# Kernel optimization log

Hardware: AMD Instinct MI355X
Metric: run time of the kernel (lower is better)

The kernel has to match this reference:

```python
import jax, jax.numpy as jnp
import numpy as np

N, E, G = 50000, 800000, 128   # nodes, edges, graphs per batch
IN, HID, OUT = 128, 256, 10
EPS = 1e-5


def setup_inputs() -> dict:
    key = jax.random.key(0)
    ks = jax.random.split(key, 12)

    def w(k, shape, fan_in):
        return jax.random.normal(k, shape, jnp.float32) * np.float32(1.0 / np.sqrt(fan_in))

    H2 = HID // 2
    return {
        "n_feat": jax.random.normal(ks[0], (N, IN), jnp.float32),
        "src": jax.random.randint(ks[1], (E,), 0, N, dtype=jnp.int32),
        "dst": jax.random.randint(ks[2], (E,), 0, N, dtype=jnp.int32),
        "graph_ids": jnp.sort(jax.random.randint(ks[3], (N,), 0, G, dtype=jnp.int32)),
        "W1": w(ks[4], (IN, HID), IN), "b1": jnp.zeros((HID,), jnp.float32),
        "W2": w(ks[5], (HID, H2), HID), "b2": jnp.zeros((H2,), jnp.float32),
        "W3": w(ks[6], (H2, H2), H2), "b3": jnp.zeros((H2,), jnp.float32),
        "Wf1": w(ks[7], (H2, H2), H2), "bf1": jnp.zeros((H2,), jnp.float32),
        "Wf2": w(ks[8], (H2, OUT), H2), "bf2": jnp.zeros((OUT,), jnp.float32),
        "gamma": jnp.ones((H2,), jnp.float32),
        "beta": jnp.zeros((H2,), jnp.float32),
    }


def _graph_conv(x, W, b, src, dst, out_dis, in_dis):
    # DGL GraphConv, norm='both': D_dst^{-1/2} A D_src^{-1/2} X W + b
    h = x * out_dis[:, None]                                   # [N, d]
    agg = jax.ops.segment_sum(h[src], dst, num_segments=N)     # scatter-add over edges
    agg = agg * in_dis[:, None]
    return agg @ W + b


def reference(n_feat, src, dst, graph_ids,
              W1, b1, W2, b2, W3, b3, Wf1, bf1, Wf2, bf2, gamma, beta):
    ones_e = jnp.ones((E,), jnp.float32)
    out_deg = jax.ops.segment_sum(ones_e, src, num_segments=N)
    in_deg = jax.ops.segment_sum(ones_e, dst, num_segments=N)
    out_dis = jax.lax.rsqrt(jnp.clip(out_deg, 1.0))   # degree clamped to min 1
    in_dis = jax.lax.rsqrt(jnp.clip(in_deg, 1.0))

    x = jax.nn.relu(_graph_conv(n_feat, W1, b1, src, dst, out_dis, in_dis))
    x = jax.nn.relu(_graph_conv(x, W2, b2, src, dst, out_dis, in_dis))
    x = jax.nn.relu(_graph_conv(x, W3, b3, src, dst, out_dis, in_dis))

    # SumPooling readout -> [G, HID//2]
    embedding = jax.ops.segment_sum(x, graph_ids, num_segments=G)

    # BatchNorm1d (training-mode batch stats, biased variance)
    mean = jnp.mean(embedding, axis=0)
    var = jnp.mean((embedding - mean) ** 2, axis=0)
    bn = (embedding - mean) * jax.lax.rsqrt(var + EPS) * gamma + beta

    h = jax.nn.relu(bn @ Wf1 + bf1)
    logits = h @ Wf2 + bf2
    return embedding, jax.nn.log_softmax(logits, axis=-1)
```

## Files before the change

### kernel.cpp

```cpp
#include <hip/hip_runtime.h>

#define N_NODES 50000
#define N_EDGES 800000
#define N_GRAPHS 128
#define IN_DIM 128
#define HID 256
#define H2 128
#define OUT_DIM 10
#define BN_EPS 1e-5f

#define NBUCK 196
#define K1_ITEMS 2048
#define NB_EDGE ((N_EDGES + K1_ITEMS - 1) / K1_ITEMS)
#define BND_BLOCKS ((N_NODES + 255) / 256)
#define CW1_BLOCKS  ((IN_DIM * HID) / 256)
#define CW2_BLOCKS  ((HID * H2) / 256)
#define CW3_BLOCKS  ((H2 * H2) / 256)

typedef __attribute__((ext_vector_type(8))) short short8_t;
typedef __attribute__((ext_vector_type(4))) float f32x4;

__device__ __forceinline__ unsigned short f2bf(float f) {
    union { float f; unsigned u; } x; x.f = f;
    unsigned r = x.u + 0x7fffu + ((x.u >> 16) & 1u);
    return (unsigned short)(r >> 16);
}
__device__ __forceinline__ float bf2f(unsigned short h) {
    union { unsigned u; float f; } x; x.u = ((unsigned)h) << 16;
    return x.f;
}
__device__ __forceinline__ unsigned pack2(float a, float b) {
    return (unsigned)f2bf(a) | ((unsigned)f2bf(b) << 16);
}

__device__ __forceinline__ void convw_body(const float* __restrict__ W,
        unsigned short* __restrict__ WT, int K, int NOUT, int i) {
    int k = i / NOUT, n = i - k * NOUT;
    WT[(size_t)n * K + k] = f2bf(W[i]);
}

__global__ __launch_bounds__(256) void k1_hist(const int* __restrict__ src,
        const int* __restrict__ dst, int* __restrict__ cntD, int* __restrict__ cntS,
        const float* __restrict__ W1, const float* __restrict__ W2, const float* __restrict__ W3,
        unsigned short* __restrict__ W1T, unsigned short* __restrict__ W2T,
        unsigned short* __restrict__ W3T,
        const int* __restrict__ gid, int* __restrict__ gstart) {
    int bid = blockIdx.x, tid = threadIdx.x;
    if (bid < NB_EDGE) {
        __shared__ int hD[256], hS[256];
        hD[tid] = 0; hS[tid] = 0;
        __syncthreads();
        int base = bid * K1_ITEMS;
#pragma unroll
        for (int it = 0; it < 8; it++) {
            int e = base + it * 256 + tid;
            if (e < N_EDGES) {
                atomicAdd(&hD[dst[e] >> 8], 1);
                atomicAdd(&hS[src[e] >> 8], 1);
            }
        }
        __syncthreads();
        cntD[bid * 256 + tid] = hD[tid];
        cntS[bid * 256 + tid] = hS[tid];
        return;
    }
    bid -= NB_EDGE;
    if (bid < CW1_BLOCKS) { convw_body(W1, W1T, IN_DIM, HID, bid * 256 + tid); return; }
    bid -= CW1_BLOCKS;
    if (bid < CW2_BLOCKS) { convw_body(W2, W2T, HID, H2, bid * 256 + tid); return; }
    bid -= CW2_BLOCKS;
    if (bid < CW3_BLOCKS) { convw_body(W3, W3T, H2, H2, bid * 256 + tid); return; }
    bid -= CW3_BLOCKS;
    {
        int n = bid * 256 + tid;
        if (n >= N_NODES) return;
        int g = gid[n];
        int gp = (n == 0) ? -1 : gid[n - 1];
        for (int k = gp + 1; k <= g; k++) gstart[k] = n;
        if (n == N_NODES - 1)
            for (int k = g + 1; k <= N_GRAPHS; k++) gstart[k] = N_NODES;
    }
}

__global__ __launch_bounds__(256) void k2_scan(const int* __restrict__ cntD,
        const int* __restrict__ cntS, int* __restrict__ offD, int* __restrict__ offS,
        int* __restrict__ baseD, int* __restrict__ baseS, int* __restrict__ rowptr) {
    int b = threadIdx.x;
    int runD = 0, runS = 0;
    for (int blk = 0; blk < NB_EDGE; blk++) {
        int cD = cntD[blk * 256 + b]; offD[blk * 256 + b] = runD; runD += cD;
        int cS = cntS[blk * 256 + b]; offS[blk * 256 + b] = runS; runS += cS;
    }
    __shared__ int ldsD[256], ldsS[256];
    ldsD[b] = runD; ldsS[b] = runS;
    __syncthreads();
    for (int off = 1; off < 256; off <<= 1) {
        int uD = (b >= off) ? ldsD[b - off] : 0;
        int uS = (b >= off) ? ldsS[b - off] : 0;
        __syncthreads();
        ldsD[b] += uD; ldsS[b] += uS;
        __syncthreads();
    }
    baseD[b] = ldsD[b] - runD;
    baseS[b] = ldsS[b] - runS;
    if (b == 0) rowptr[N_NODES] = N_EDGES;
}

__global__ __launch_bounds__(256) void k3_scatter(const int* __restrict__ src,
        const int* __restrict__ dst, const int* __restrict__ offD, const int* __restrict__ offS,
        const int* __restrict__ baseD, const int* __restrict__ baseS,
        uint2* __restrict__ bufD, int* __restrict__ bufS) {
    __shared__ int cD[256], cS[256];
    int bid = blockIdx.x, tid = threadIdx.x;
    cD[tid] = baseD[tid] + offD[bid * 256 + tid];
    cS[tid] = baseS[tid] + offS[bid * 256 + tid];
    __syncthreads();
    int base = bid * K1_ITEMS;
#pragma unroll
    for (int it = 0; it < 8; it++) {
        int e = base + it * 256 + tid;
        if (e < N_EDGES) {
            int d = dst[e], s = src[e];
            int pd = atomicAdd(&cD[d >> 8], 1);
            bufD[pd] = make_uint2((unsigned)d, (unsigned)s);
            int ps = atomicAdd(&cS[s >> 8], 1);
            bufS[ps] = s;
        }
    }
}

__global__ __launch_bounds__(256) void k4_csr(const uint2* __restrict__ bufD,
        const int* __restrict__ baseD, int* __restrict__ indeg,
        int* __restrict__ rowptr, int* __restrict__ csr_src) {
    __shared__ int cnt[256], lds[256], curs[256];
    int b = blockIdx.x, t = threadIdx.x;
    int eb = baseD[b], ee = baseD[b + 1];
    cnt[t] = 0;
    __syncthreads();
    for (int e = eb + t; e < ee; e += 256)
        atomicAdd(&cnt[bufD[e].x & 255], 1);
    __syncthreads();
    int v = cnt[t];
    lds[t] = v;
    __syncthreads();
    for (int off = 1; off < 256; off <<= 1) {
        int u = (t >= off) ? lds[t - off] : 0;
        __syncthreads();
        lds[t] += u;
        __syncthreads();
    }
    int n0 = b << 8;
    int ex = eb + lds[t] - v;
    if (n0 + t < N_NODES) {
        indeg[n0 + t] = v;
        rowptr[n0 + t] = ex;
    }
    curs[t] = ex;
    __syncthreads();
    for (int e = eb + t; e < ee; e += 256) {
        uint2 ed = bufD[e];
        int slot = atomicAdd(&curs[ed.x & 255], 1);
        csr_src[slot] = (int)ed.y;
    }
}

__global__ __launch_bounds__(256) void k5_outdeg_prescale(const int* __restrict__ bufS,
        const int* __restrict__ baseS, const float* __restrict__ n_feat,
        int* __restrict__ outdeg, unsigned int* __restrict__ Xs) {
    __shared__ int cnt[256];
    __shared__ float od[256];
    int b = blockIdx.x, t = threadIdx.x;
    int eb = baseS[b], ee = baseS[b + 1];
    cnt[t] = 0;
    __syncthreads();
    for (int e = eb + t; e < ee; e += 256)
        atomicAdd(&cnt[bufS[e] & 255], 1);
    __syncthreads();
    int n0 = b << 8;
    int nn = min(256, N_NODES - n0);
    if (t < nn) outdeg[n0 + t] = cnt[t];
    od[t] = rsqrtf(fmaxf((float)cnt[t], 1.0f));
    __syncthreads();
    int pc = t & 127;
    int rh = t >> 7;
    for (int r = rh; r < nn; r += 2) {
        int row = n0 + r;
        float2 v = *reinterpret_cast<const float2*>(n_feat + (size_t)row * 128 + pc * 2);
        float s = od[r];
        Xs[(size_t)row * 64 + pc] = pack2(v.x * s, v.y * s);
    }
}

template<int MODE>
__global__ __launch_bounds__(256) void pull_agg(const unsigned int* __restrict__ X,
        const int* __restrict__ rowptr, const int* __restrict__ csr_src,
        const int* __restrict__ indeg, const int* __restrict__ outdeg,
        const float* __restrict__ bias, unsigned int* __restrict__ out) {
    int lane = threadIdx.x & 63;
    int n = blockIdx.x * 4 + (threadIdx.x >> 6);
    n = __builtin_amdgcn_readfirstlane(n);
    if (n >= N_NODES) return;
    int l32 = lane & 31;
    int half = lane >> 5;
    int beg = rowptr[n];
    int cnt = rowptr[n + 1] - beg;
    const int* ep = csr_src + beg;
    float a0 = 0.f, a1 = 0.f, a2 = 0.f, a3 = 0.f;
    int voff = l32 << 1;

    auto acc = [&](uint2 u) {
        a0 += bf2f((unsigned short)(u.x & 0xffff));
        a1 += bf2f((unsigned short)(u.x >> 16));
        a2 += bf2f((unsigned short)(u.y & 0xffff));
        a3 += bf2f((unsigned short)(u.y >> 16));
    };

    int j = 0;
    for (; j + 8 <= cnt; j += 8) {
        uint2 u[4];
#pragma unroll
        for (int q = 0; q < 4; q++) {
            int sa = ep[j + 2 * q], sb = ep[j + 2 * q + 1];
            int s = half ? sb : sa;
            u[q] = *reinterpret_cast<const uint2*>(X + ((size_t)s << 6) + voff);
        }
#pragma unroll
        for (int q = 0; q < 4; q++) acc(u[q]);
    }
    for (; j + 2 <= cnt; j += 2) {
        int sa = ep[j], sb = ep[j + 1];
        int s = half ? sb : sa;
        acc(*reinterpret_cast<const uint2*>(X + ((size_t)s << 6) + voff));
    }
    if (j < cnt && half == 0) {
        int s = ep[j];
        acc(*reinterpret_cast<const uint2*>(X + ((size_t)s << 6) + voff));
    }

    a0 += __shfl_xor(a0, 32);
    a1 += __shfl_xor(a1, 32);
    a2 += __shfl_xor(a2, 32);
    a3 += __shfl_xor(a3, 32);

    if (lane < 32) {
        float id = rsqrtf(fmaxf((float)indeg[n], 1.0f));
        float v0 = a0 * id, v1 = a1 * id, v2 = a2 * id, v3 = a3 * id;
        if (MODE == 1) {
            float odv = rsqrtf(fmaxf((float)outdeg[n], 1.0f));
            float4 bv = *reinterpret_cast<const float4*>(bias + l32 * 4);
            v0 = fmaxf(v0 + bv.x, 0.f) * odv;
            v1 = fmaxf(v1 + bv.y, 0.f) * odv;
            v2 = fmaxf(v2 + bv.z, 0.f) * odv;
            v3 = fmaxf(v3 + bv.w, 0.f) * odv;
        }
        uint2 o = make_uint2(pack2(v0, v1), pack2(v2, v3));
        *reinterpret_cast<uint2*>(out + (size_t)n * 64 + voff) = o;
    }
}

template<int K, int NOUT, int EPI>
__global__ __launch_bounds__(256) void mfma_gemm(const unsigned short* __restrict__ A,
        const unsigned short* __restrict__ WT, const float* __restrict__ aux,
        const int* __restrict__ auxi, unsigned short* __restrict__ out) {
    constexpr int KK  = K / 32;
    constexpr int NBW = NOUT / 64;
    int wave = threadIdx.x >> 6;
    int lane = threadIdx.x & 63;
    int col0 = lane & 15;
    int kgrp = (lane >> 4) * 8;
    int wcol = wave * NBW * 16;

    short8_t b[NBW][KK];
    {
        const unsigned short* wbase = WT + (size_t)(wcol + col0) * K + kgrp;
#pragma unroll
        for (int n = 0; n < NBW; n++)
#pragma unroll
            for (int kk = 0; kk < KK; kk++)
                b[n][kk] = *reinterpret_cast<const short8_t*>(
                    wbase + (size_t)n * 16 * K + kk * 32);
    }
    float bv[NBW];
    if (EPI == 1) {
#pragma unroll
        for (int n = 0; n < NBW; n++) bv[n] = aux[wcol + n * 16 + col0];
    }

    constexpr int NT = N_NODES / 16;
    for (int rt = blockIdx.x; rt < NT; rt += gridDim.x) {
        const unsigned short* ap = A + (size_t)(rt * 16 + col0) * K + kgrp;
        short8_t a[KK];
#pragma unroll
        for (int kk = 0; kk < KK; kk++)
            a[kk] = *reinterpret_cast<const short8_t*>(ap + kk * 32);

        f32x4 acc[NBW];
#pragma unroll
        for (int n = 0; n < NBW; n++) acc[n] = f32x4{0.f, 0.f, 0.f, 0.f};
#pragma unroll
        for (int kk = 0; kk < KK; kk++)
#pragma unroll
            for (int n = 0; n < NBW; n++)
                acc[n] = __builtin_amdgcn_mfma_f32_16x16x32_bf16(a[kk], b[n][kk], acc[n], 0, 0, 0);

        int rbase = rt * 16 + ((lane >> 4) << 2);
        float rs[4];
        if (EPI == 2) {
#pragma unroll
            for (int j = 0; j < 4; j++)
                rs[j] = rsqrtf(fmaxf((float)auxi[rbase + j], 1.0f));
        }
#pragma unroll
        for (int n = 0; n < NBW; n++) {
            int col = wcol + n * 16 + col0;
#pragma unroll
            for (int j = 0; j < 4; j++) {
                float v = acc[n][j];
                if (EPI == 1) v = fmaxf(v + bv[n], 0.f);
                if (EPI == 2) v = v * rs[j];
                out[(size_t)(rbase + j) * NOUT + col] = f2bf(v);
            }
        }
    }
}

__global__ __launch_bounds__(512) void seg_pool(const unsigned int* __restrict__ X,
        const int* __restrict__ gstart, float* __restrict__ emb) {
    int g = blockIdx.x;
    int lane = threadIdx.x & 63;
    int stripe = threadIdx.x >> 6;
    int beg = gstart[g], end = gstart[g + 1];
    float ax = 0.f, ay = 0.f;
    for (int r = beg + stripe; r < end; r += 8) {
        unsigned u = X[(size_t)r * 64 + lane];
        ax += bf2f((unsigned short)(u & 0xffff));
        ay += bf2f((unsigned short)(u >> 16));
    }
    __shared__ float bufx[8][64], bufy[8][64];
    bufx[stripe][lane] = ax;
    bufy[stripe][lane] = ay;
    __syncthreads();
    if (stripe == 0) {
        float sx = 0.f, sy = 0.f;
#pragma unroll
        for (int q = 0; q < 8; q++) { sx += bufx[q][lane]; sy += bufy[q][lane]; }
        emb[g * 128 + lane * 2]     = sx;
        emb[g * 128 + lane * 2 + 1] = sy;
    }
}

__global__ __launch_bounds__(128) void fc_kernel(const float* __restrict__ emb,
        const float* __restrict__ gamma, const float* __restrict__ beta,
        const float* __restrict__ Wf1, const float* __restrict__ bf1,
        const float* __restrict__ Wf2, const float* __restrict__ bf2,
        float* __restrict__ out_ls) {
    __shared__ float h[H2];
    __shared__ float logits[OUT_DIM];
    int g = blockIdx.x;
    int j = threadIdx.x;
    float s = 0.f;
    for (int q = 0; q < N_GRAPHS; q++) s += emb[q * 128 + j];
    float mean = s * (1.0f / N_GRAPHS);
    float v = 0.f;
    for (int q = 0; q < N_GRAPHS; q++) {
        float d = emb[q * 128 + j] - mean;
        v += d * d;
    }
    v *= (1.0f / N_GRAPHS);
    float scale = rsqrtf(v + BN_EPS) * gamma[j];
    h[j] = (emb[g * 128 + j] - mean) * scale + beta[j];
    __syncthreads();
    float acc = bf1[j];
    for (int k = 0; k < H2; k++) acc += h[k] * Wf1[k * H2 + j];
    __syncthreads();
    h[j] = fmaxf(acc, 0.f);
    __syncthreads();
    if (j < OUT_DIM) {
        float a2 = bf2[j];
        for (int k = 0; k < H2; k++) a2 += h[k] * Wf2[k * OUT_DIM + j];
        logits[j] = a2;
    }
    __syncthreads();
    if (j < OUT_DIM) {
        float m = -1e30f;
        for (int o = 0; o < OUT_DIM; o++) m = fmaxf(m, logits[o]);
        float se = 0.f;
        for (int o = 0; o < OUT_DIM; o++) se += expf(logits[o] - m);
        out_ls[g * OUT_DIM + j] = logits[j] - m - logf(se);
    }
}

extern "C" void kernel_launch(void* const* d_in, const int* in_sizes, int n_in,
                              void* d_out, int out_size, void* d_ws, size_t ws_size,
                              hipStream_t stream) {
    const float* n_feat = (const float*)d_in[0];
    const int*   src    = (const int*)d_in[1];
    const int*   dst    = (const int*)d_in[2];
    const int*   gid    = (const int*)d_in[3];
    const float* W1     = (const float*)d_in[4];
    const float* b1     = (const float*)d_in[5];
    const float* W2     = (const float*)d_in[6];
    const float* b2     = (const float*)d_in[7];
    const float* W3     = (const float*)d_in[8];
    const float* b3     = (const float*)d_in[9];
    const float* Wf1    = (const float*)d_in[10];
    const float* bf1    = (const float*)d_in[11];
    const float* Wf2    = (const float*)d_in[12];
    const float* bf2    = (const float*)d_in[13];
    const float* gamma  = (const float*)d_in[14];
    const float* beta   = (const float*)d_in[15];
    float* out = (float*)d_out;

    char* ws = (char*)d_ws;
    size_t off = 0;
    auto alloc = [&](size_t bytes) {
        void* p = ws + off;
        off = (off + bytes + 255) & ~(size_t)255;
        return p;
    };
    int* cntD    = (int*)alloc((size_t)NB_EDGE * 256 * 4);
    int* cntS    = (int*)alloc((size_t)NB_EDGE * 256 * 4);
    int* offD    = (int*)alloc((size_t)NB_EDGE * 256 * 4);
    int* offS    = (int*)alloc((size_t)NB_EDGE * 256 * 4);
    int* baseD   = (int*)alloc(257 * 4);
    int* baseS   = (int*)alloc(257 * 4);
    int* indeg   = (int*)alloc((size_t)N_NODES * 4);
    int* outdeg  = (int*)alloc((size_t)N_NODES * 4);
    int* rowptr  = (int*)alloc((size_t)(N_NODES + 1) * 4);
    int* gstart  = (int*)alloc((size_t)(N_GRAPHS + 1) * 4);
    uint2* bufD  = (uint2*)alloc((size_t)N_EDGES * 8);
    int* bufS    = (int*)alloc((size_t)N_EDGES * 4);
    int* csr_src = (int*)alloc((size_t)N_EDGES * 4);
    unsigned short* Xs  = (unsigned short*)alloc((size_t)N_NODES * 128 * 2);
    unsigned short* A   = (unsigned short*)alloc((size_t)N_NODES * 128 * 2);
    unsigned short* B   = (unsigned short*)alloc((size_t)N_NODES * 256 * 2);
    unsigned short* W1T = (unsigned short*)alloc((size_t)IN_DIM * HID * 2);
    unsigned short* W2T = (unsigned short*)alloc((size_t)HID * H2 * 2);
    unsigned short* W3T = (unsigned short*)alloc((size_t)H2 * H2 * 2);

    k1_hist<<<NB_EDGE + CW1_BLOCKS + CW2_BLOCKS + CW3_BLOCKS + BND_BLOCKS, 256, 0, stream>>>(
        src, dst, cntD, cntS, W1, W2, W3, W1T, W2T, W3T, gid, gstart);
    k2_scan<<<1, 256, 0, stream>>>(cntD, cntS, offD, offS, baseD, baseS, rowptr);
    k3_scatter<<<NB_EDGE, 256, 0, stream>>>(src, dst, offD, offS, baseD, baseS, bufD, bufS);
    k4_csr<<<NBUCK, 256, 0, stream>>>(bufD, baseD, indeg, rowptr, csr_src);
    k5_outdeg_prescale<<<NBUCK, 256, 0, stream>>>(bufS, baseS, n_feat, outdeg,
                                                  (unsigned int*)Xs);

    const int AGG_GRID = (N_NODES + 3) / 4;
    const int GEMM_GRID = 1024;

    pull_agg<0><<<AGG_GRID, 256, 0, stream>>>((unsigned int*)Xs, rowptr, csr_src,
                                              indeg, outdeg, nullptr, (unsigned int*)A);
    mfma_gemm<128, 256, 1><<<GEMM_GRID, 256, 0, stream>>>(A, W1T, b1, nullptr, B);

    mfma_gemm<256, 128, 2><<<GEMM_GRID, 256, 0, stream>>>(B, W2T, nullptr, outdeg, A);
    pull_agg<1><<<AGG_GRID, 256, 0, stream>>>((unsigned int*)A, rowptr, csr_src,
                                              indeg, outdeg, b2, (unsigned int*)B);

    pull_agg<0><<<AGG_GRID, 256, 0, stream>>>((unsigned int*)B, rowptr, csr_src,
                                              indeg, outdeg, nullptr, (unsigned int*)A);
    mfma_gemm<128, 128, 1><<<GEMM_GRID, 256, 0, stream>>>(A, W3T, b3, nullptr, B);

    seg_pool<<<N_GRAPHS, 512, 0, stream>>>((unsigned int*)B, gstart, out);
    fc_kernel<<<N_GRAPHS, 128, 0, stream>>>(out, gamma, beta, Wf1, bf1, Wf2, bf2,
                                            out + (size_t)N_GRAPHS * H2);
}
```

Measured before the change: 265.2 us.

## Split pull aggregation by feature quarter with persistent grid; keep final layer fp32

The pull aggregation kernel now makes each block handle one quarter of the 128 feature columns, using a persistent grid of 2048 blocks that strides over nodes. Each wave gathers 8 edges at a time with 8 lanes per edge and reduces across lanes with shuffles. Block index bits assign quarters so that neighbouring blocks share column slices, which is meant to improve cache locality of the gathered rows. The last GEMM also writes fp32 output that the pooling kernel reads directly, removing one bf16 rounding step at the cost of twice the bytes written and read.

New measurement: 353.8 us. 1.33x slower.

```diff
diff --git a/kernel.cpp b/kernel.cpp
--- a/kernel.cpp
+++ b/kernel.cpp
@@ -196,72 +196,81 @@
         const int* __restrict__ rowptr, const int* __restrict__ csr_src,
         const int* __restrict__ indeg, const int* __restrict__ outdeg,
         const float* __restrict__ bias, unsigned int* __restrict__ out) {
+    int b = blockIdx.x;
+    int q = (b & 7) >> 1;
+    int wave = threadIdx.x >> 6;
     int lane = threadIdx.x & 63;
-    int n = blockIdx.x * 4 + (threadIdx.x >> 6);
-    n = __builtin_amdgcn_readfirstlane(n);
-    if (n >= N_NODES) return;
-    int l32 = lane & 31;
-    int half = lane >> 5;
-    int beg = rowptr[n];
-    int cnt = rowptr[n + 1] - beg;
-    const int* ep = csr_src + beg;
-    float a0 = 0.f, a1 = 0.f, a2 = 0.f, a3 = 0.f;
-    int voff = l32 << 1;
-
-    auto acc = [&](uint2 u) {
-        a0 += bf2f((unsigned short)(u.x & 0xffff));
-        a1 += bf2f((unsigned short)(u.x >> 16));
-        a2 += bf2f((unsigned short)(u.y & 0xffff));
-        a3 += bf2f((unsigned short)(u.y >> 16));
-    };
-
-    int j = 0;
-    for (; j + 8 <= cnt; j += 8) {
-        uint2 u[4];
-#pragma unroll
-        for (int q = 0; q < 4; q++) {
-            int sa = ep[j + 2 * q], sb = ep[j + 2 * q + 1];
-            int s = half ? sb : sa;
-            u[q] = *reinterpret_cast<const uint2*>(X + ((size_t)s << 6) + voff);
-        }
-#pragma unroll
-        for (int q = 0; q < 4; q++) acc(u[q]);
-    }
-    for (; j + 2 <= cnt; j += 2) {
-        int sa = ep[j], sb = ep[j + 1];
-        int s = half ? sb : sa;
-        acc(*reinterpret_cast<const uint2*>(X + ((size_t)s << 6) + voff));
-    }
-    if (j < cnt && half == 0) {
-        int s = ep[j];
-        acc(*reinterpret_cast<const uint2*>(X + ((size_t)s << 6) + voff));
-    }
-
-    a0 += __shfl_xor(a0, 32);
-    a1 += __shfl_xor(a1, 32);
-    a2 += __shfl_xor(a2, 32);
-    a3 += __shfl_xor(a3, 32);
-
-    if (lane < 32) {
-        float id = rsqrtf(fmaxf((float)indeg[n], 1.0f));
-        float v0 = a0 * id, v1 = a1 * id, v2 = a2 * id, v3 = a3 * id;
-        if (MODE == 1) {
-            float odv = rsqrtf(fmaxf((float)outdeg[n], 1.0f));
-            float4 bv = *reinterpret_cast<const float4*>(bias + l32 * 4);
-            v0 = fmaxf(v0 + bv.x, 0.f) * odv;
-            v1 = fmaxf(v1 + bv.y, 0.f) * odv;
-            v2 = fmaxf(v2 + bv.z, 0.f) * odv;
-            v3 = fmaxf(v3 + bv.w, 0.f) * odv;
-        }
-        uint2 o = make_uint2(pack2(v0, v1), pack2(v2, v3));
-        *reinterpret_cast<uint2*>(out + (size_t)n * 64 + voff) = o;
-    }
-}
-
-template<int K, int NOUT, int EPI>
+    int eslot = lane >> 3;
+    int c8 = lane & 7;
+    int qoff = q * 16 + c8 * 2;
+
+    int wid_in_q = (b >> 3) * 2 + (b & 1);
+    int nstride = (gridDim.x >> 2) * 4;
+
+    for (int n0 = wid_in_q * 4 + wave; n0 < N_NODES; n0 += nstride) {
+        int n = __builtin_amdgcn_readfirstlane(n0);
+        int beg = rowptr[n];
+        int cnt = rowptr[n + 1] - beg;
+        const int* ep = csr_src + beg;
+        float a0 = 0.f, a1 = 0.f, a2 = 0.f, a3 = 0.f;
+
+        int j = 0;
+        for (; j + 32 <= cnt; j += 32) {
+            uint2 u[4];
+#pragma unroll
+            for (int t = 0; t < 4; t++) {
+                int s = ep[j + t * 8 + eslot];
+                u[t] = *reinterpret_cast<const uint2*>(X + ((size_t)s << 6) + qoff);
+            }
+#pragma unroll
+            for (int t = 0; t < 4; t++) {
+                a0 += bf2f((unsigned short)(u[t].x & 0xffff));
+                a1 += bf2f((unsigned short)(u[t].x >> 16));
+                a2 += bf2f((unsigned short)(u[t].y & 0xffff));
+                a3 += bf2f((unsigned short)(u[t].y >> 16));
+            }
+        }
+        for (; j < cnt; j += 8) {
+            int jj = j + eslot;
+            int s = ep[min(jj, cnt - 1)];
+            uint2 u = *reinterpret_cast<const uint2*>(X + ((size_t)s << 6) + qoff);
+            if (jj < cnt) {
+                a0 += bf2f((unsigned short)(u.x & 0xffff));
+                a1 += bf2f((unsigned short)(u.x >> 16));
+                a2 += bf2f((unsigned short)(u.y & 0xffff));
+                a3 += bf2f((unsigned short)(u.y >> 16));
+            }
+        }
+
+#pragma unroll
+        for (int d = 8; d < 64; d <<= 1) {
+            a0 += __shfl_xor(a0, d);
+            a1 += __shfl_xor(a1, d);
+            a2 += __shfl_xor(a2, d);
+            a3 += __shfl_xor(a3, d);
+        }
+
+        if (eslot == 0) {
+            float id = rsqrtf(fmaxf((float)indeg[n], 1.0f));
+            float v0 = a0 * id, v1 = a1 * id, v2 = a2 * id, v3 = a3 * id;
+            if (MODE == 1) {
+                float odv = rsqrtf(fmaxf((float)outdeg[n], 1.0f));
+                float4 bv = *reinterpret_cast<const float4*>(bias + q * 32 + c8 * 4);
+                v0 = fmaxf(v0 + bv.x, 0.f) * odv;
+                v1 = fmaxf(v1 + bv.y, 0.f) * odv;
+                v2 = fmaxf(v2 + bv.z, 0.f) * odv;
+                v3 = fmaxf(v3 + bv.w, 0.f) * odv;
+            }
+            uint2 o = make_uint2(pack2(v0, v1), pack2(v2, v3));
+            *reinterpret_cast<uint2*>(out + (size_t)n * 64 + qoff) = o;
+        }
+    }
+}
+
+template<int K, int NOUT, int EPI, bool F32OUT>
 __global__ __launch_bounds__(256) void mfma_gemm(const unsigned short* __restrict__ A,
         const unsigned short* __restrict__ WT, const float* __restrict__ aux,
-        const int* __restrict__ auxi, unsigned short* __restrict__ out) {
+        const int* __restrict__ auxi, void* __restrict__ outv) {
     constexpr int KK  = K / 32;
     constexpr int NBW = NOUT / 64;
     int wave = threadIdx.x >> 6;
@@ -318,13 +327,16 @@
                 float v = acc[n][j];
                 if (EPI == 1) v = fmaxf(v + bv[n], 0.f);
                 if (EPI == 2) v = v * rs[j];
-                out[(size_t)(rbase + j) * NOUT + col] = f2bf(v);
-            }
-        }
-    }
-}
-
-__global__ __launch_bounds__(512) void seg_pool(const unsigned int* __restrict__ X,
+                if (F32OUT)
+                    ((float*)outv)[(size_t)(rbase + j) * NOUT + col] = v;
+                else
+                    ((unsigned short*)outv)[(size_t)(rbase + j) * NOUT + col] = f2bf(v);
+            }
+        }
+    }
+}
+
+__global__ __launch_bounds__(512) void seg_pool(const float* __restrict__ X,
         const int* __restrict__ gstart, float* __restrict__ emb) {
     int g = blockIdx.x;
     int lane = threadIdx.x & 63;
@@ -332,9 +344,8 @@
     int beg = gstart[g], end = gstart[g + 1];
     float ax = 0.f, ay = 0.f;
     for (int r = beg + stripe; r < end; r += 8) {
-        unsigned u = X[(size_t)r * 64 + lane];
-        ax += bf2f((unsigned short)(u & 0xffff));
-        ay += bf2f((unsigned short)(u >> 16));
+        float2 v = *reinterpret_cast<const float2*>(X + (size_t)r * 128 + lane * 2);
+        ax += v.x; ay += v.y;
     }
     __shared__ float bufx[8][64], bufy[8][64];
     bufx[stripe][lane] = ax;
@@ -437,6 +448,7 @@
     unsigned short* W1T = (unsigned short*)alloc((size_t)IN_DIM * HID * 2);
     unsigned short* W2T = (unsigned short*)alloc((size_t)HID * H2 * 2);
     unsigned short* W3T = (unsigned short*)alloc((size_t)H2 * H2 * 2);
+    float* Bf32 = (float*)B;
 
     k1_hist<<<NB_EDGE + CW1_BLOCKS + CW2_BLOCKS + CW3_BLOCKS + BND_BLOCKS, 256, 0, stream>>>(
         src, dst, cntD, cntS, W1, W2, W3, W1T, W2T, W3T, gid, gstart);
@@ -446,22 +458,22 @@
     k5_outdeg_prescale<<<NBUCK, 256, 0, stream>>>(bufS, baseS, n_feat, outdeg,
                                                   (unsigned int*)Xs);
 
-    const int AGG_GRID = (N_NODES + 3) / 4;
+    const int AGG_GRID = 2048;
     const int GEMM_GRID = 1024;
 
     pull_agg<0><<<AGG_GRID, 256, 0, stream>>>((unsigned int*)Xs, rowptr, csr_src,
                                               indeg, outdeg, nullptr, (unsigned int*)A);
-    mfma_gemm<128, 256, 1><<<GEMM_GRID, 256, 0, stream>>>(A, W1T, b1, nullptr, B);
-
-    mfma_gemm<256, 128, 2><<<GEMM_GRID, 256, 0, stream>>>(B, W2T, nullptr, outdeg, A);
+    mfma_gemm<128, 256, 1, false><<<GEMM_GRID, 256, 0, stream>>>(A, W1T, b1, nullptr, B);
+
+    mfma_gemm<256, 128, 2, false><<<GEMM_GRID, 256, 0, stream>>>(B, W2T, nullptr, outdeg, A);
     pull_agg<1><<<AGG_GRID, 256, 0, stream>>>((unsigned int*)A, rowptr, csr_src,
                                               indeg, outdeg, b2, (unsigned int*)B);
 
     pull_agg<0><<<AGG_GRID, 256, 0, stream>>>((unsigned int*)B, rowptr, csr_src,
                                               indeg, outdeg, nullptr, (unsigned int*)A);
-    mfma_gemm<128, 128, 1><<<GEMM_GRID, 256, 0, stream>>>(A, W3T, b3, nullptr, B);
-
-    seg_pool<<<N_GRAPHS, 512, 0, stream>>>((unsigned int*)B, gstart, out);
+    mfma_gemm<128, 128, 1, true><<<GEMM_GRID, 256, 0, stream>>>(A, W3T, b3, nullptr, Bf32);
+
+    seg_pool<<<N_GRAPHS, 512, 0, stream>>>(Bf32, gstart, out);
     fc_kernel<<<N_GRAPHS, 128, 0, stream>>>(out, gamma, beta, Wf1, bf1, Wf2, bf2,
                                             out + (size_t)N_GRAPHS * H2);
 }
```
